# Kernel optimization log

Measured on AMD Instinct MI355X. Metric: run time of the kernel, lower is better.

## Reference

```python
import jax, jax.numpy as jnp
import numpy as np

# ODEBlock integrates dy/dt = f(t, y) from T0 to T1 with the dopri5 (Dormand-Prince RK45)
# stage structure. torchdiffeq's dopri5 is adaptive; for a jit/vjp-friendly reference we
# run the same 6-stage dopri5 tableau with a fixed number of steps (same per-step math).
T0, T1 = 0.0, 1.0
NUM_STEPS = 16

BATCH, D, H = 512, 1024, 2048


def setup_inputs() -> dict:
    key = jax.random.key(0)
    k0, k1, k2 = jax.random.split(key, 3)
    x = jax.random.normal(k0, (BATCH, D), dtype=jnp.float32)
    W1 = jax.random.normal(k1, (D, H), dtype=jnp.float32) / np.float32(np.sqrt(D))
    b1 = jnp.zeros((H,), dtype=jnp.float32)
    W2 = jax.random.normal(k2, (H, D), dtype=jnp.float32) / np.float32(np.sqrt(H))
    b2 = jnp.zeros((D,), dtype=jnp.float32)
    return {"x": x, "W1": W1, "b1": b1, "W2": W2, "b2": b2}


def reference(x, W1, b1, W2, b2):
    def f(t, y):
        # odefunc: 2-layer tanh MLP, autonomous in t
        return jnp.tanh(y @ W1 + b1) @ W2 + b2

    h = jnp.float32((T1 - T0) / NUM_STEPS)

    def step(carry, _):
        y, t = carry
        k1 = f(t, y)
        k2 = f(t + h * (1.0 / 5.0), y + h * (1.0 / 5.0) * k1)
        k3 = f(t + h * (3.0 / 10.0), y + h * ((3.0 / 40.0) * k1 + (9.0 / 40.0) * k2))
        k4 = f(t + h * (4.0 / 5.0),
               y + h * ((44.0 / 45.0) * k1 - (56.0 / 15.0) * k2 + (32.0 / 9.0) * k3))
        k5 = f(t + h * (8.0 / 9.0),
               y + h * ((19372.0 / 6561.0) * k1 - (25360.0 / 2187.0) * k2
                        + (64448.0 / 6561.0) * k3 - (212.0 / 729.0) * k4))
        k6 = f(t + h,
               y + h * ((9017.0 / 3168.0) * k1 - (355.0 / 33.0) * k2
                        + (46732.0 / 5247.0) * k3 + (49.0 / 176.0) * k4
                        - (5103.0 / 18656.0) * k5))
        # 5th-order solution weights (b7 = 0, so k7/FSAL not needed for the update)
        y_next = y + h * ((35.0 / 384.0) * k1 + (500.0 / 1113.0) * k3
                          + (125.0 / 192.0) * k4 - (2187.0 / 6784.0) * k5
                          + (11.0 / 84.0) * k6)
        return (y_next, t + h), None

    (y_final, _), _ = jax.lax.scan(step, (x, jnp.float32(T0)), None, length=NUM_STEPS)
    return y_final
```

## Files before the change

### kernel.cpp

```cpp
#include <hip/hip_runtime.h>
#include <hip/hip_bf16.h>

using bf16 = __hip_bfloat16;
typedef __attribute__((ext_vector_type(8))) short short8;
typedef __attribute__((ext_vector_type(4))) float f32x4;
typedef __attribute__((ext_vector_type(16))) float f32x16;
typedef __attribute__((ext_vector_type(4))) unsigned short u16x4;

#define MFMA32(A, B, C) __builtin_amdgcn_mfma_f32_32x32x16_bf16(A, B, C, 0, 0, 0)

constexpr int Mdim = 512;
constexpr int Ddim = 1024;
constexpr int Hdim = 2048;
constexpr size_t MH = (size_t)Mdim * Hdim;
constexpr size_t KPL4 = MH / 4;

constexpr double Hs = 1.0 / 16.0;
constexpr float CF[6][6] = {
    {float(Hs * 1 / 5.), 0.f, 0.f, 0.f, 0.f, 0.f},
    {float(Hs * 3 / 40.), float(Hs * 9 / 40.), 0.f, 0.f, 0.f, 0.f},
    {float(Hs * 44 / 45.), float(-Hs * 56 / 15.), float(Hs * 32 / 9.), 0.f, 0.f, 0.f},
    {float(Hs * 19372 / 6561.), float(-Hs * 25360 / 2187.), float(Hs * 64448 / 6561.),
     float(-Hs * 212 / 729.), 0.f, 0.f},
    {float(Hs * 9017 / 3168.), float(-Hs * 355 / 33.), float(Hs * 46732 / 5247.),
     float(Hs * 49 / 176.), float(-Hs * 5103 / 18656.), 0.f},
    {float(Hs * 35 / 384.), 0.f, float(Hs * 500 / 1113.), float(Hs * 125 / 192.),
     float(-Hs * 2187 / 6784.), float(Hs * 11 / 84.)},
};

__device__ __forceinline__ float tanh_fast(float x) {
  float xc = fminf(fmaxf(x, -15.0f), 15.0f);
  float t = __expf(2.0f * xc);
  return (t - 1.0f) * __builtin_amdgcn_rcpf(t + 1.0f);
}

__device__ __forceinline__ unsigned short f2bf(float x) {
  bf16 b = __float2bfloat16(x);
  return *(unsigned short*)&b;
}
__device__ __forceinline__ float bf2f(unsigned short u) {
  bf16 b = *(bf16*)&u;
  return __bfloat162float(b);
}

__device__ __forceinline__ void gload_lds16(const void* g, void* lds) {
  __builtin_amdgcn_global_load_lds((const __attribute__((address_space(1))) void*)g,
                                   (__attribute__((address_space(3))) void*)lds, 16, 0, 0);
}

enum { M_PLAIN = 0, M_INIT = 1, M_STG = 2, M_FINAL = 3 };

struct GArgs {
  const bf16* A;
  const bf16* Bt;
  const float* b1;
  const float* b2w1;
  const float* xin;
  const float* b2;
  float* yW1;
  bf16* T;
  bf16* K;
  float* G;
  bf16* Wout;
  float* y;
};

template <int MODE, int STAGE, int NDIM, int KDIM>
__global__ __launch_bounds__(512, 2) void fused_gemm(GArgs a) {
  constexpr int BK = 128;
  constexpr int NITER = KDIM / BK;
  constexpr int NP = (NDIM / 64) / 8;

  extern __shared__ char smem_c[];

  const int tid = threadIdx.x;
  const int lane = tid & 63;
  const int wid = tid >> 6;
  const int l31 = lane & 31;
  const int hi = lane >> 5;

  const int bid = blockIdx.x;
  const int nt = (bid & 7) * NP + ((bid >> 3) % NP);
  const int mt = (bid >> 3) / NP;
  const int brow = mt * 64, bcol = nt * 64;
  const int tile = mt * (NDIM / 64) + nt;

  const int rs0 = tid >> 4;
  const int cgS = (tid & 15) ^ (rs0 & 7);
  const bf16* pA0 = a.A + (size_t)(brow + rs0) * KDIM + cgS * 8;
  const bf16* pA1 = pA0 + (size_t)32 * KDIM;
  const bf16* pB0 = a.Bt + (size_t)(bcol + rs0) * KDIM + cgS * 8;
  const bf16* pB1 = pB0 + (size_t)32 * KDIM;
  char* dA = smem_c + tid * 16;
  char* dB = smem_c + 16384 + tid * 16;

#define STAGE_TILE(T_)                                                       \
  {                                                                          \
    const int B_ = ((T_) % 3) * 32768;                                       \
    const int KO_ = (T_)*BK;                                                 \
    gload_lds16(pA0 + KO_, dA + B_); gload_lds16(pA1 + KO_, dA + B_ + 8192); \
    gload_lds16(pB0 + KO_, dB + B_); gload_lds16(pB1 + KO_, dB + B_ + 8192); \
  }

  const int xo = l31 * 256 + (((wid * 2 + hi) ^ (l31 & 7)) << 4);
  const char* rA = smem_c + xo;
  const char* rB = smem_c + 16384 + xo;

  f32x16 acc[2][2] = {};

  STAGE_TILE(0)
  STAGE_TILE(1)

#pragma unroll
  for (int t = 0; t < NITER; ++t) {
    if (t < NITER - 1) asm volatile("s_waitcnt vmcnt(4)" ::: "memory");
    else               asm volatile("s_waitcnt vmcnt(0)" ::: "memory");
    __builtin_amdgcn_s_barrier();
    __builtin_amdgcn_sched_barrier(0);
    if (t + 2 < NITER) STAGE_TILE(t + 2)
    const int BO = (t % 3) * 32768;
    short8 af0 = *(const short8*)(rA + BO);
    short8 af1 = *(const short8*)(rA + BO + 8192);
    short8 bw0 = *(const short8*)(rB + BO);
    short8 bw1 = *(const short8*)(rB + BO + 8192);
    __builtin_amdgcn_s_setprio(1);
    acc[0][0] = MFMA32(af0, bw0, acc[0][0]);
    acc[0][1] = MFMA32(af0, bw1, acc[0][1]);
    acc[1][0] = MFMA32(af1, bw0, acc[1][0]);
    acc[1][1] = MFMA32(af1, bw1, acc[1][1]);
    __builtin_amdgcn_s_setprio(0);
  }
#undef STAGE_TILE

  __syncthreads();
#pragma unroll
  for (int mf = 0; mf < 2; ++mf)
#pragma unroll
    for (int nf = 0; nf < 2; ++nf)
#pragma unroll
      for (int g = 0; g < 4; ++g) {
        f32x4 v = {acc[mf][nf][g * 4 + 0], acc[mf][nf][g * 4 + 1],
                   acc[mf][nf][g * 4 + 2], acc[mf][nf][g * 4 + 3]};
        *(f32x4*)(smem_c + ((((mf * 2 + nf) * 4 + g) * 8 + wid) << 10) + lane * 16) = v;
      }
  __syncthreads();

#pragma unroll
  for (int of = 0; of < 2; ++of) {
    const int q = wid * 2 + of;
    f32x4 s = {};
#pragma unroll
    for (int w = 0; w < 8; ++w)
      s += *(const f32x4*)(smem_c + (((q * 8 + w) << 10)) + lane * 16);

    const int p = q >> 2, g = q & 3;
    const int mf = p >> 1, nf = p & 1;
    const int c = bcol + nf * 32 + l31;
    const int r0 = brow + mf * 32 + g * 8 + hi * 4;
    if constexpr (MODE == M_PLAIN) {
#pragma unroll
      for (int e = 0; e < 4; ++e) a.Wout[(size_t)(r0 + e) * NDIM + c] = __float2bfloat16(s[e]);
    } else if constexpr (MODE == M_INIT) {
      ((f32x4*)a.yW1)[(size_t)(tile * 16 + q) * 64 + lane] = s;
      const float bv = a.b1[c];
#pragma unroll
      for (int e = 0; e < 4; ++e) {
        const size_t idx = (size_t)(r0 + e) * NDIM + c;
        const float tv = tanh_fast(s[e] + bv);
        a.T[idx] = __float2bfloat16(tv);
        a.G[idx] = CF[5][0] * tv;
      }
    } else if constexpr (MODE == M_STG) {
      u16x4* Kq = (u16x4*)a.K;
      const size_t kb = (size_t)(tile * 16 + q) * 64 + lane;
      const float bb = a.b2w1[c];
      float Kv[4], comb[4];
      const f32x4 yv = ((const f32x4*)a.yW1)[kb];
#pragma unroll
      for (int e = 0; e < 4; ++e) Kv[e] = s[e] + bb;
      if constexpr (STAGE <= 5) {
        u16x4 kw;
#pragma unroll
        for (int e = 0; e < 4; ++e) kw[e] = f2bf(Kv[e]);
        Kq[(size_t)(STAGE - 1) * KPL4 + kb] = kw;
      }
#pragma unroll
      for (int e = 0; e < 4; ++e) comb[e] = yv[e] + CF[STAGE - 1][STAGE - 1] * Kv[e];
      if constexpr (STAGE > 1 && CF[STAGE - 1][0] != 0.f) {
        u16x4 kj = Kq[0 * KPL4 + kb];
#pragma unroll
        for (int e = 0; e < 4; ++e) comb[e] += CF[STAGE - 1][0] * bf2f(kj[e]);
      }
      if constexpr (STAGE > 2 && CF[STAGE - 1][1] != 0.f) {
        u16x4 kj = Kq[1 * KPL4 + kb];
#pragma unroll
        for (int e = 0; e < 4; ++e) comb[e] += CF[STAGE - 1][1] * bf2f(kj[e]);
      }
      if constexpr (STAGE > 3 && CF[STAGE - 1][2] != 0.f) {
        u16x4 kj = Kq[2 * KPL4 + kb];
#pragma unroll
        for (int e = 0; e < 4; ++e) comb[e] += CF[STAGE - 1][2] * bf2f(kj[e]);
      }
      if constexpr (STAGE > 4 && CF[STAGE - 1][3] != 0.f) {
        u16x4 kj = Kq[3 * KPL4 + kb];
#pragma unroll
        for (int e = 0; e < 4; ++e) comb[e] += CF[STAGE - 1][3] * bf2f(kj[e]);
      }
      if constexpr (STAGE > 5 && CF[STAGE - 1][4] != 0.f) {
        u16x4 kj = Kq[4 * KPL4 + kb];
#pragma unroll
        for (int e = 0; e < 4; ++e) comb[e] += CF[STAGE - 1][4] * bf2f(kj[e]);
      }
      if constexpr (STAGE == 6) {
        f32x4 cw = {comb[0], comb[1], comb[2], comb[3]};
        ((f32x4*)a.yW1)[kb] = cw;
      }
      const float bv = a.b1[c];
#pragma unroll
      for (int e = 0; e < 4; ++e) {
        const size_t idx = (size_t)(r0 + e) * NDIM + c;
        const float tv = tanh_fast(comb[e] + bv);
        a.T[idx] = __float2bfloat16(tv);
        if constexpr (STAGE < 6) {
          if constexpr (CF[5][STAGE] != 0.f) a.G[idx] += CF[5][STAGE] * tv;
        } else {
          a.G[idx] += CF[5][0] * tv;
        }
      }
    } else {
      const float bv = a.b2[c];
#pragma unroll
      for (int e = 0; e < 4; ++e) {
        const size_t idx = (size_t)(r0 + e) * NDIM + c;
        a.y[idx] = a.xin[idx] + s[e] + bv;
      }
    }
  }
}

__global__ void transpose_to_bf16(const float* __restrict__ in, bf16* __restrict__ out, int R,
                                  int C) {
  __shared__ float t[32][33];
  const int c0 = blockIdx.x * 32, r0 = blockIdx.y * 32;
#pragma unroll
  for (int i = threadIdx.y; i < 32; i += 8)
    t[i][threadIdx.x] = in[(size_t)(r0 + i) * C + c0 + threadIdx.x];
  __syncthreads();
#pragma unroll
  for (int i = threadIdx.y; i < 32; i += 8)
    out[(size_t)(c0 + i) * R + r0 + threadIdx.x] = __float2bfloat16(t[threadIdx.x][i]);
}

__global__ void cast_bf16(const float* __restrict__ in, bf16* __restrict__ out, int n4) {
  int i = blockIdx.x * 256 + threadIdx.x;
  if (i < n4) {
    float4 v = *(const float4*)(in + i * 4);
    bf16* o = out + i * 4;
    o[0] = __float2bfloat16(v.x); o[1] = __float2bfloat16(v.y);
    o[2] = __float2bfloat16(v.z); o[3] = __float2bfloat16(v.w);
  }
}

__global__ void b2w1_kernel(const float* __restrict__ b2, const float* __restrict__ W1,
                            float* __restrict__ out) {
  const int h = blockIdx.x * 256 + threadIdx.x;
  float s = 0.f;
  for (int d = 0; d < Ddim; ++d) s += b2[d] * W1[(size_t)d * Hdim + h];
  out[h] = s;
}

extern "C" void kernel_launch(void* const* d_in, const int* in_sizes, int n_in, void* d_out,
                              int out_size, void* d_ws, size_t ws_size, hipStream_t stream) {
  const float* x = (const float*)d_in[0];
  const float* W1 = (const float*)d_in[1];
  const float* b1 = (const float*)d_in[2];
  const float* W2 = (const float*)d_in[3];
  const float* b2 = (const float*)d_in[4];
  float* y = (float*)d_out;

  char* ws = (char*)d_ws;
  bf16* W1t = (bf16*)(ws + 0);
  bf16* W2bf = (bf16*)(ws + (4ull << 20));
  bf16* W2t = (bf16*)(ws + (8ull << 20));
  bf16* W21t = (bf16*)(ws + (12ull << 20));
  bf16* xbf = (bf16*)(ws + (20ull << 20));
  bf16* Tbuf = (bf16*)(ws + (21ull << 20));
  bf16* Kbuf = (bf16*)(ws + (23ull << 20));
  bf16* Gbf = (bf16*)(ws + (33ull << 20));
  float* yW1 = (float*)(ws + (35ull << 20));
  float* Gacc = (float*)(ws + (39ull << 20));
  float* b2w1 = (float*)(ws + (43ull << 20));

  GArgs a = {};
  a.b1 = b1; a.b2w1 = b2w1; a.xin = x; a.b2 = b2;
  a.yW1 = yW1; a.T = Tbuf; a.K = Kbuf; a.G = Gacc; a.y = y;

  constexpr int SMEM = 131072;
  hipFuncSetAttribute((const void*)&fused_gemm<M_PLAIN, 0, Hdim, 1024>,
                      hipFuncAttributeMaxDynamicSharedMemorySize, SMEM);
  hipFuncSetAttribute((const void*)&fused_gemm<M_INIT, 0, Hdim, 1024>,
                      hipFuncAttributeMaxDynamicSharedMemorySize, SMEM);
  hipFuncSetAttribute((const void*)&fused_gemm<M_STG, 1, Hdim, Hdim>,
                      hipFuncAttributeMaxDynamicSharedMemorySize, SMEM);
  hipFuncSetAttribute((const void*)&fused_gemm<M_STG, 2, Hdim, Hdim>,
                      hipFuncAttributeMaxDynamicSharedMemorySize, SMEM);
  hipFuncSetAttribute((const void*)&fused_gemm<M_STG, 3, Hdim, Hdim>,
                      hipFuncAttributeMaxDynamicSharedMemorySize, SMEM);
  hipFuncSetAttribute((const void*)&fused_gemm<M_STG, 4, Hdim, Hdim>,
                      hipFuncAttributeMaxDynamicSharedMemorySize, SMEM);
  hipFuncSetAttribute((const void*)&fused_gemm<M_STG, 5, Hdim, Hdim>,
                      hipFuncAttributeMaxDynamicSharedMemorySize, SMEM);
  hipFuncSetAttribute((const void*)&fused_gemm<M_STG, 6, Hdim, Hdim>,
                      hipFuncAttributeMaxDynamicSharedMemorySize, SMEM);
  hipFuncSetAttribute((const void*)&fused_gemm<M_FINAL, 0, Ddim, Hdim>,
                      hipFuncAttributeMaxDynamicSharedMemorySize, SMEM);

  transpose_to_bf16<<<dim3(Hdim / 32, Ddim / 32), dim3(32, 8), 0, stream>>>(W1, W1t, Ddim, Hdim);
  transpose_to_bf16<<<dim3(Ddim / 32, Hdim / 32), dim3(32, 8), 0, stream>>>(W2, W2t, Hdim, Ddim);
  cast_bf16<<<(Hdim * Ddim / 4 + 255) / 256, 256, 0, stream>>>(W2, W2bf, Hdim * Ddim / 4);
  cast_bf16<<<(Mdim * Ddim / 4 + 255) / 256, 256, 0, stream>>>(x, xbf, Mdim * Ddim / 4);
  b2w1_kernel<<<Hdim / 256, 256, 0, stream>>>(b2, W1, b2w1);

  {
    GArgs p = a; p.A = W1t; p.Bt = W2bf; p.Wout = W21t;
    fused_gemm<M_PLAIN, 0, Hdim, 1024><<<32 * 32, 512, SMEM, stream>>>(p);
  }
  {
    GArgs p = a; p.A = xbf; p.Bt = W1t;
    fused_gemm<M_INIT, 0, Hdim, 1024><<<8 * 32, 512, SMEM, stream>>>(p);
  }

  GArgs sg = a; sg.A = Tbuf; sg.Bt = W21t;
  for (int step = 0; step < 16; ++step) {
    fused_gemm<M_STG, 1, Hdim, Hdim><<<8 * 32, 512, SMEM, stream>>>(sg);
    fused_gemm<M_STG, 2, Hdim, Hdim><<<8 * 32, 512, SMEM, stream>>>(sg);
    fused_gemm<M_STG, 3, Hdim, Hdim><<<8 * 32, 512, SMEM, stream>>>(sg);
    fused_gemm<M_STG, 4, Hdim, Hdim><<<8 * 32, 512, SMEM, stream>>>(sg);
    fused_gemm<M_STG, 5, Hdim, Hdim><<<8 * 32, 512, SMEM, stream>>>(sg);
    if (step < 15)
      fused_gemm<M_STG, 6, Hdim, Hdim><<<8 * 32, 512, SMEM, stream>>>(sg);
  }

  cast_bf16<<<(int)(MH / 4 + 255) / 256, 256, 0, stream>>>(Gacc, Gbf, (int)(MH / 4));
  {
    GArgs p = a; p.A = Gbf; p.Bt = W2t;
    fused_gemm<M_FINAL, 0, Ddim, Hdim><<<8 * 16, 512, SMEM, stream>>>(p);
  }
}
```

Baseline: 1.358 ms.

## Add dedicated stage GEMM kernel with prepacked W21 fragments loaded directly to registers

Adds a specialized per-stage kernel that streams only the activation tile through LDS via a triple-buffered global_load_lds pipeline. The weight operand W21 is repacked once into MFMA fragment order so each wave loads its B fragments straight from global memory into registers. A split-K reduction across the 8 waves through shared memory then feeds the unchanged stage epilogue. The aim is to cut LDS traffic and staging cost for B in the 95 hot stage launches, at the price of an extra packing pass, more workspace, and uncoalesced-per-block register loads of the weights.

```diff
diff --git a/kernel.cpp b/kernel.cpp
--- a/kernel.cpp
+++ b/kernel.cpp
@@ -53,6 +53,7 @@
 struct GArgs {
   const bf16* A;
   const bf16* Bt;
+  const bf16* Bp;
   const float* b1;
   const float* b2w1;
   const float* xin;
@@ -64,6 +65,164 @@
   bf16* Wout;
   float* y;
 };
+
+template <int STAGE>
+__device__ __forceinline__ void stage_epilogue(const GArgs& a, f32x4 s, int tile, int q,
+                                               int lane, int r0, int c, int NDIM) {
+  u16x4* Kq = (u16x4*)a.K;
+  const size_t kb = (size_t)(tile * 16 + q) * 64 + lane;
+  const float bb = a.b2w1[c];
+  float Kv[4], comb[4];
+  const f32x4 yv = ((const f32x4*)a.yW1)[kb];
+#pragma unroll
+  for (int e = 0; e < 4; ++e) Kv[e] = s[e] + bb;
+  if constexpr (STAGE <= 5) {
+    u16x4 kw;
+#pragma unroll
+    for (int e = 0; e < 4; ++e) kw[e] = f2bf(Kv[e]);
+    Kq[(size_t)(STAGE - 1) * KPL4 + kb] = kw;
+  }
+#pragma unroll
+  for (int e = 0; e < 4; ++e) comb[e] = yv[e] + CF[STAGE - 1][STAGE - 1] * Kv[e];
+  if constexpr (STAGE > 1 && CF[STAGE - 1][0] != 0.f) {
+    u16x4 kj = Kq[0 * KPL4 + kb];
+#pragma unroll
+    for (int e = 0; e < 4; ++e) comb[e] += CF[STAGE - 1][0] * bf2f(kj[e]);
+  }
+  if constexpr (STAGE > 2 && CF[STAGE - 1][1] != 0.f) {
+    u16x4 kj = Kq[1 * KPL4 + kb];
+#pragma unroll
+    for (int e = 0; e < 4; ++e) comb[e] += CF[STAGE - 1][1] * bf2f(kj[e]);
+  }
+  if constexpr (STAGE > 3 && CF[STAGE - 1][2] != 0.f) {
+    u16x4 kj = Kq[2 * KPL4 + kb];
+#pragma unroll
+    for (int e = 0; e < 4; ++e) comb[e] += CF[STAGE - 1][2] * bf2f(kj[e]);
+  }
+  if constexpr (STAGE > 4 && CF[STAGE - 1][3] != 0.f) {
+    u16x4 kj = Kq[3 * KPL4 + kb];
+#pragma unroll
+    for (int e = 0; e < 4; ++e) comb[e] += CF[STAGE - 1][3] * bf2f(kj[e]);
+  }
+  if constexpr (STAGE > 5 && CF[STAGE - 1][4] != 0.f) {
+    u16x4 kj = Kq[4 * KPL4 + kb];
+#pragma unroll
+    for (int e = 0; e < 4; ++e) comb[e] += CF[STAGE - 1][4] * bf2f(kj[e]);
+  }
+  if constexpr (STAGE == 6) {
+    f32x4 cw = {comb[0], comb[1], comb[2], comb[3]};
+    ((f32x4*)a.yW1)[kb] = cw;
+  }
+  const float bv = a.b1[c];
+#pragma unroll
+  for (int e = 0; e < 4; ++e) {
+    const size_t idx = (size_t)(r0 + e) * NDIM + c;
+    const float tv = tanh_fast(comb[e] + bv);
+    a.T[idx] = __float2bfloat16(tv);
+    if constexpr (STAGE < 6) {
+      if constexpr (CF[5][STAGE] != 0.f) a.G[idx] += CF[5][STAGE] * tv;
+    } else {
+      a.G[idx] += CF[5][0] * tv;
+    }
+  }
+}
+
+template <int STAGE>
+__global__ __launch_bounds__(512, 2) void fused_stage(GArgs a) {
+  constexpr int NITER = 16;
+  extern __shared__ char smem_c[];
+
+  const int tid = threadIdx.x;
+  const int lane = tid & 63;
+  const int wid = tid >> 6;
+  const int l31 = lane & 31;
+  const int hi = lane >> 5;
+
+  const int bid = blockIdx.x;
+  const int nt = (bid & 7) * 4 + ((bid >> 3) & 3);
+  const int mt = bid >> 5;
+  const int brow = mt * 64, bcol = nt * 64;
+  const int tile = mt * 32 + nt;
+
+  const int rs0 = tid >> 4;
+  const int cgS = (tid & 15) ^ (rs0 & 7);
+  const bf16* pA0 = a.A + (size_t)(brow + rs0) * 2048 + cgS * 8;
+  const bf16* pA1 = pA0 + (size_t)32 * 2048;
+  char* dA = smem_c + tid * 16;
+
+#define STG_A(T_)                                                              \
+  {                                                                            \
+    const int B_ = ((T_) % 3) * 16384;                                         \
+    const int KO_ = (T_)*128;                                                  \
+    gload_lds16(pA0 + KO_, dA + B_); gload_lds16(pA1 + KO_, dA + B_ + 8192);   \
+  }
+
+  const bf16* bp0 = a.Bp + ((size_t)(nt * 2) * 128 + wid) * 512 + lane * 8;
+  const bf16* bp1 = bp0 + (size_t)128 * 512;
+
+  const int xo = l31 * 256 + (((wid * 2 + hi) ^ (l31 & 7)) << 4);
+  const char* rA = smem_c + xo;
+
+  f32x16 acc[2][2] = {};
+  short8 bB[3][2];
+
+  bB[0][0] = *(const short8*)(bp0);
+  bB[0][1] = *(const short8*)(bp1);
+  STG_A(0)
+  bB[1][0] = *(const short8*)(bp0 + 4096);
+  bB[1][1] = *(const short8*)(bp1 + 4096);
+  STG_A(1)
+
+#pragma unroll
+  for (int t = 0; t < NITER; ++t) {
+    if (t < NITER - 1) asm volatile("s_waitcnt vmcnt(4)" ::: "memory");
+    else               asm volatile("s_waitcnt vmcnt(0)" ::: "memory");
+    __builtin_amdgcn_s_barrier();
+    __builtin_amdgcn_sched_barrier(0);
+    if (t + 2 < NITER) {
+      bB[(t + 2) % 3][0] = *(const short8*)(bp0 + (t + 2) * 4096);
+      bB[(t + 2) % 3][1] = *(const short8*)(bp1 + (t + 2) * 4096);
+      STG_A(t + 2)
+    }
+    const int BO = (t % 3) * 16384;
+    short8 af0 = *(const short8*)(rA + BO);
+    short8 af1 = *(const short8*)(rA + BO + 8192);
+    __builtin_amdgcn_s_setprio(1);
+    acc[0][0] = MFMA32(af0, bB[t % 3][0], acc[0][0]);
+    acc[0][1] = MFMA32(af0, bB[t % 3][1], acc[0][1]);
+    acc[1][0] = MFMA32(af1, bB[t % 3][0], acc[1][0]);
+    acc[1][1] = MFMA32(af1, bB[t % 3][1], acc[1][1]);
+    __builtin_amdgcn_s_setprio(0);
+  }
+#undef STG_A
+
+  __syncthreads();
+#pragma unroll
+  for (int mf = 0; mf < 2; ++mf)
+#pragma unroll
+    for (int nf = 0; nf < 2; ++nf)
+#pragma unroll
+      for (int g = 0; g < 4; ++g) {
+        f32x4 v = {acc[mf][nf][g * 4 + 0], acc[mf][nf][g * 4 + 1],
+                   acc[mf][nf][g * 4 + 2], acc[mf][nf][g * 4 + 3]};
+        *(f32x4*)(smem_c + ((((mf * 2 + nf) * 4 + g) * 8 + wid) << 10) + lane * 16) = v;
+      }
+  __syncthreads();
+
+#pragma unroll
+  for (int of = 0; of < 2; ++of) {
+    const int q = wid * 2 + of;
+    f32x4 s = {};
+#pragma unroll
+    for (int w = 0; w < 8; ++w)
+      s += *(const f32x4*)(smem_c + (((q * 8 + w) << 10)) + lane * 16);
+    const int p = q >> 2, g = q & 3;
+    const int mf = p >> 1, nf = p & 1;
+    const int c = bcol + nf * 32 + l31;
+    const int r0 = brow + mf * 32 + g * 8 + hi * 4;
+    stage_epilogue<STAGE>(a, s, tile, q, lane, r0, c, Hdim);
+  }
+}
 
 template <int MODE, int STAGE, int NDIM, int KDIM>
 __global__ __launch_bounds__(512, 2) void fused_gemm(GArgs a) {
@@ -170,63 +329,6 @@
         a.T[idx] = __float2bfloat16(tv);
         a.G[idx] = CF[5][0] * tv;
       }
-    } else if constexpr (MODE == M_STG) {
-      u16x4* Kq = (u16x4*)a.K;
-      const size_t kb = (size_t)(tile * 16 + q) * 64 + lane;
-      const float bb = a.b2w1[c];
-      float Kv[4], comb[4];
-      const f32x4 yv = ((const f32x4*)a.yW1)[kb];
-#pragma unroll
-      for (int e = 0; e < 4; ++e) Kv[e] = s[e] + bb;
-      if constexpr (STAGE <= 5) {
-        u16x4 kw;
-#pragma unroll
-        for (int e = 0; e < 4; ++e) kw[e] = f2bf(Kv[e]);
-        Kq[(size_t)(STAGE - 1) * KPL4 + kb] = kw;
-      }
-#pragma unroll
-      for (int e = 0; e < 4; ++e) comb[e] = yv[e] + CF[STAGE - 1][STAGE - 1] * Kv[e];
-      if constexpr (STAGE > 1 && CF[STAGE - 1][0] != 0.f) {
-        u16x4 kj = Kq[0 * KPL4 + kb];
-#pragma unroll
-        for (int e = 0; e < 4; ++e) comb[e] += CF[STAGE - 1][0] * bf2f(kj[e]);
-      }
-      if constexpr (STAGE > 2 && CF[STAGE - 1][1] != 0.f) {
-        u16x4 kj = Kq[1 * KPL4 + kb];
-#pragma unroll
-        for (int e = 0; e < 4; ++e) comb[e] += CF[STAGE - 1][1] * bf2f(kj[e]);
-      }
-      if constexpr (STAGE > 3 && CF[STAGE - 1][2] != 0.f) {
-        u16x4 kj = Kq[2 * KPL4 + kb];
-#pragma unroll
-        for (int e = 0; e < 4; ++e) comb[e] += CF[STAGE - 1][2] * bf2f(kj[e]);
-      }
-      if constexpr (STAGE > 4 && CF[STAGE - 1][3] != 0.f) {
-        u16x4 kj = Kq[3 * KPL4 + kb];
-#pragma unroll
-        for (int e = 0; e < 4; ++e) comb[e] += CF[STAGE - 1][3] * bf2f(kj[e]);
-      }
-      if constexpr (STAGE > 5 && CF[STAGE - 1][4] != 0.f) {
-        u16x4 kj = Kq[4 * KPL4 + kb];
-#pragma unroll
-        for (int e = 0; e < 4; ++e) comb[e] += CF[STAGE - 1][4] * bf2f(kj[e]);
-      }
-      if constexpr (STAGE == 6) {
-        f32x4 cw = {comb[0], comb[1], comb[2], comb[3]};
-        ((f32x4*)a.yW1)[kb] = cw;
-      }
-      const float bv = a.b1[c];
-#pragma unroll
-      for (int e = 0; e < 4; ++e) {
-        const size_t idx = (size_t)(r0 + e) * NDIM + c;
-        const float tv = tanh_fast(comb[e] + bv);
-        a.T[idx] = __float2bfloat16(tv);
-        if constexpr (STAGE < 6) {
-          if constexpr (CF[5][STAGE] != 0.f) a.G[idx] += CF[5][STAGE] * tv;
-        } else {
-          a.G[idx] += CF[5][0] * tv;
-        }
-      }
     } else {
       const float bv = a.b2[c];
 #pragma unroll
@@ -236,6 +338,15 @@
       }
     }
   }
+}
+
+__global__ void pack_w21(const bf16* __restrict__ in, bf16* __restrict__ out) {
+  const int t = blockIdx.x * 256 + threadIdx.x;
+  const int lane = t & 63;
+  const int kk = (t >> 6) & 127;
+  const int nt32 = t >> 13;
+  const bf16* src = in + (size_t)(nt32 * 32 + (lane & 31)) * 2048 + kk * 16 + (lane >> 5) * 8;
+  *(short8*)(out + (size_t)t * 8) = *(const short8*)src;
 }
 
 __global__ void transpose_to_bf16(const float* __restrict__ in, bf16* __restrict__ out, int R,
@@ -290,30 +401,31 @@
   float* yW1 = (float*)(ws + (35ull << 20));
   float* Gacc = (float*)(ws + (39ull << 20));
   float* b2w1 = (float*)(ws + (43ull << 20));
+  bf16* W21p = (bf16*)(ws + (44ull << 20));
 
   GArgs a = {};
   a.b1 = b1; a.b2w1 = b2w1; a.xin = x; a.b2 = b2;
-  a.yW1 = yW1; a.T = Tbuf; a.K = Kbuf; a.G = Gacc; a.y = y;
+  a.yW1 = yW1; a.T = Tbuf; a.K = Kbuf; a.G = Gacc; a.y = y; a.Bp = W21p;
 
   constexpr int SMEM = 131072;
   hipFuncSetAttribute((const void*)&fused_gemm<M_PLAIN, 0, Hdim, 1024>,
                       hipFuncAttributeMaxDynamicSharedMemorySize, SMEM);
   hipFuncSetAttribute((const void*)&fused_gemm<M_INIT, 0, Hdim, 1024>,
                       hipFuncAttributeMaxDynamicSharedMemorySize, SMEM);
-  hipFuncSetAttribute((const void*)&fused_gemm<M_STG, 1, Hdim, Hdim>,
-                      hipFuncAttributeMaxDynamicSharedMemorySize, SMEM);
-  hipFuncSetAttribute((const void*)&fused_gemm<M_STG, 2, Hdim, Hdim>,
-                      hipFuncAttributeMaxDynamicSharedMemorySize, SMEM);
-  hipFuncSetAttribute((const void*)&fused_gemm<M_STG, 3, Hdim, Hdim>,
-                      hipFuncAttributeMaxDynamicSharedMemorySize, SMEM);
-  hipFuncSetAttribute((const void*)&fused_gemm<M_STG, 4, Hdim, Hdim>,
-                      hipFuncAttributeMaxDynamicSharedMemorySize, SMEM);
-  hipFuncSetAttribute((const void*)&fused_gemm<M_STG, 5, Hdim, Hdim>,
-                      hipFuncAttributeMaxDynamicSharedMemorySize, SMEM);
-  hipFuncSetAttribute((const void*)&fused_gemm<M_STG, 6, Hdim, Hdim>,
-                      hipFuncAttributeMaxDynamicSharedMemorySize, SMEM);
   hipFuncSetAttribute((const void*)&fused_gemm<M_FINAL, 0, Ddim, Hdim>,
                       hipFuncAttributeMaxDynamicSharedMemorySize, SMEM);
+  hipFuncSetAttribute((const void*)&fused_stage<1>, hipFuncAttributeMaxDynamicSharedMemorySize,
+                      SMEM);
+  hipFuncSetAttribute((const void*)&fused_stage<2>, hipFuncAttributeMaxDynamicSharedMemorySize,
+                      SMEM);
+  hipFuncSetAttribute((const void*)&fused_stage<3>, hipFuncAttributeMaxDynamicSharedMemorySize,
+                      SMEM);
+  hipFuncSetAttribute((const void*)&fused_stage<4>, hipFuncAttributeMaxDynamicSharedMemorySize,
+                      SMEM);
+  hipFuncSetAttribute((const void*)&fused_stage<5>, hipFuncAttributeMaxDynamicSharedMemorySize,
+                      SMEM);
+  hipFuncSetAttribute((const void*)&fused_stage<6>, hipFuncAttributeMaxDynamicSharedMemorySize,
+                      SMEM);
 
   transpose_to_bf16<<<dim3(Hdim / 32, Ddim / 32), dim3(32, 8), 0, stream>>>(W1, W1t, Ddim, Hdim);
   transpose_to_bf16<<<dim3(Ddim / 32, Hdim / 32), dim3(32, 8), 0, stream>>>(W2, W2t, Hdim, Ddim);
@@ -325,20 +437,21 @@
     GArgs p = a; p.A = W1t; p.Bt = W2bf; p.Wout = W21t;
     fused_gemm<M_PLAIN, 0, Hdim, 1024><<<32 * 32, 512, SMEM, stream>>>(p);
   }
+  pack_w21<<<64 * 128 * 64 / 256, 256, 0, stream>>>(W21t, W21p);
   {
     GArgs p = a; p.A = xbf; p.Bt = W1t;
     fused_gemm<M_INIT, 0, Hdim, 1024><<<8 * 32, 512, SMEM, stream>>>(p);
   }
 
-  GArgs sg = a; sg.A = Tbuf; sg.Bt = W21t;
+  GArgs sg = a; sg.A = Tbuf;
   for (int step = 0; step < 16; ++step) {
-    fused_gemm<M_STG, 1, Hdim, Hdim><<<8 * 32, 512, SMEM, stream>>>(sg);
-    fused_gemm<M_STG, 2, Hdim, Hdim><<<8 * 32, 512, SMEM, stream>>>(sg);
-    fused_gemm<M_STG, 3, Hdim, Hdim><<<8 * 32, 512, SMEM, stream>>>(sg);
-    fused_gemm<M_STG, 4, Hdim, Hdim><<<8 * 32, 512, SMEM, stream>>>(sg);
-    fused_gemm<M_STG, 5, Hdim, Hdim><<<8 * 32, 512, SMEM, stream>>>(sg);
+    fused_stage<1><<<256, 512, SMEM, stream>>>(sg);
+    fused_stage<2><<<256, 512, SMEM, stream>>>(sg);
+    fused_stage<3><<<256, 512, SMEM, stream>>>(sg);
+    fused_stage<4><<<256, 512, SMEM, stream>>>(sg);
+    fused_stage<5><<<256, 512, SMEM, stream>>>(sg);
     if (step < 15)
-      fused_gemm<M_STG, 6, Hdim, Hdim><<<8 * 32, 512, SMEM, stream>>>(sg);
+      fused_stage<6><<<256, 512, SMEM, stream>>>(sg);
   }
 
   cast_bf16<<<(int)(MH / 4 + 255) / 256, 256, 0, stream>>>(Gacc, Gbf, (int)(MH / 4));
```

After: 1.489 ms. 9.7% more time.
